# Optimization experiments

Measured on AMD Instinct MI355X. Metric: run time of the kernel, lower is better.

## Reference

```python
import jax, jax.numpy as jnp
import numpy as np

N_NODES = 100000
N_EDGES = 1_600_000
F_IN, HID, N_CLS = 128, 64, 32
NEG_SLOPE = 0.2  # PyG GATv2Conv default


def _segment_softmax(scores, seg, num_segments):
    # numerically stable softmax over edges grouped by destination node
    m = jax.ops.segment_max(scores, seg, num_segments=num_segments)
    ex = jnp.exp(scores - m[seg])
    s = jax.ops.segment_sum(ex, seg, num_segments=num_segments)
    return ex / (s[seg] + 1e-16)


def _gatv2_layer(x, src, dst, Wl, bl, Wr, br, att, bias, num_nodes):
    xl = x @ Wl + bl              # source transform  [N, C]
    xr = x @ Wr + br              # target transform  [N, C]
    # per-edge GATv2 attention logit: a . leaky_relu(xl_j + xr_i)
    e = jax.nn.leaky_relu(xl[src] + xr[dst], NEG_SLOPE) @ att  # [E]
    alpha = _segment_softmax(e, dst, num_nodes)                 # [E]
    out = jax.ops.segment_sum(alpha[:, None] * xl[src], dst, num_segments=num_nodes)
    return out + bias


def _add_self_loops(edge_index, n):
    loops = jnp.arange(n, dtype=edge_index.dtype)
    return jnp.concatenate([edge_index, jnp.stack([loops, loops])], axis=1)


def setup_inputs() -> dict:
    key = jax.random.key(0)
    ks = jax.random.split(key, 8)
    s1 = 1.0 / np.sqrt(F_IN)
    s2 = 1.0 / np.sqrt(HID)
    return {
        "x": jax.random.normal(ks[0], (N_NODES, F_IN), jnp.float32),
        "edge_index": jax.random.randint(ks[1], (2, N_EDGES), 0, N_NODES, jnp.int64),
        "W1l": jax.random.normal(ks[2], (F_IN, HID), jnp.float32) * s1,
        "b1l": jnp.zeros((HID,), jnp.float32),
        "W1r": jax.random.normal(ks[3], (F_IN, HID), jnp.float32) * s1,
        "b1r": jnp.zeros((HID,), jnp.float32),
        "att1": jax.random.normal(ks[4], (HID,), jnp.float32) * s2,
        "bias1": jnp.zeros((HID,), jnp.float32),
        "W2l": jax.random.normal(ks[5], (HID, N_CLS), jnp.float32) * s2,
        "b2l": jnp.zeros((N_CLS,), jnp.float32),
        "W2r": jax.random.normal(ks[6], (HID, N_CLS), jnp.float32) * s2,
        "b2r": jnp.zeros((N_CLS,), jnp.float32),
        "att2": jax.random.normal(ks[7], (N_CLS,), jnp.float32) / np.sqrt(N_CLS),
        "bias2": jnp.zeros((N_CLS,), jnp.float32),
    }


def reference(x, edge_index, W1l, b1l, W1r, b1r, att1, bias1,
              W2l, b2l, W2r, b2r, att2, bias2):
    n = x.shape[0]
    ei = _add_self_loops(edge_index, n)
    src, dst = ei[0], ei[1]
    h = jax.nn.relu(_gatv2_layer(x, src, dst, W1l, b1l, W1r, b1r, att1, bias1, n))
    # F.dropout(training=False) is identity in eval mode
    out = _gatv2_layer(h, src, dst, W2l, b2l, W2r, b2r, att2, bias2, n)
    return out
```

## Files before the change

kernel.cpp:

```cpp
#include <hip/hip_runtime.h>
#include <hip/hip_fp16.h>
#include <math.h>

#define F_IN 128
#define HID 64
#define NCLS 32
#define NEG 0.2f
#define NBKT 128
#define BSH 7
#define BMSK 127
#define CHUNK 4096

using bf8 = __attribute__((ext_vector_type(8))) short;
using f4v = __attribute__((ext_vector_type(4))) float;
typedef _Float16 hv2 __attribute__((ext_vector_type(2)));

__device__ __forceinline__ void f4fma(float4& a, float s, const float4& w) {
    a.x = fmaf(s, w.x, a.x);
    a.y = fmaf(s, w.y, a.y);
    a.z = fmaf(s, w.z, a.z);
    a.w = fmaf(s, w.w, a.w);
}
__device__ __forceinline__ unsigned short f2bf(float f) {
    unsigned u = __float_as_uint(f);
    return (unsigned short)((u + 0x7FFFu + ((u >> 16) & 1u)) >> 16);
}
__device__ __forceinline__ unsigned short f2h(float f) {
    return __half_as_ushort(__float2half(f));
}
__device__ __forceinline__ float h2f(unsigned short u) {
    return __half2float(__ushort_as_half(u));
}
__device__ __forceinline__ unsigned pkaddabs(unsigned a, unsigned b) {
    hv2 r = __builtin_bit_cast(hv2, a) + __builtin_bit_cast(hv2, b);
    return __builtin_bit_cast(unsigned, r) & 0x7FFF7FFFu;
}
__device__ __forceinline__ float fdot2(unsigned a, unsigned b, float c) {
    return __builtin_amdgcn_fdot2(__builtin_bit_cast(hv2, a),
                                  __builtin_bit_cast(hv2, b), c, false);
}
__device__ __forceinline__ float h2lo(unsigned a) {
    return (float)__builtin_bit_cast(hv2, a).x;
}
__device__ __forceinline__ float h2hi(unsigned a) {
    return (float)__builtin_bit_cast(hv2, a).y;
}
template <int CTRL>
__device__ __forceinline__ float dpp_add(float v) {
    int t = __builtin_amdgcn_update_dpp(0, __float_as_int(v), CTRL, 0xf, 0xf, true);
    return v + __int_as_float(t);
}


__global__ __launch_bounds__(256) void bucketHist(const int* __restrict__ ei,
                                                  int Eorig, int Etot,
                                                  int* __restrict__ bucketSize, int BK) {
    __shared__ int h[1024];
    int t = threadIdx.x;
    for (int j = t; j < BK; j += 256) h[j] = 0;
    __syncthreads();
    int base = blockIdx.x * CHUNK;
    int end = base + CHUNK < Etot ? base + CHUNK : Etot;
    for (int i = base + t; i < end; i += 256) {
        int dst = i < Eorig ? ei[Eorig + i] : i - Eorig;
        atomicAdd(&h[dst >> BSH], 1);
    }
    __syncthreads();
    for (int j = t; j < BK; j += 256)
        if (h[j]) atomicAdd(&bucketSize[j], h[j]);
}

__global__ __launch_bounds__(256) void bucketScan(const int* __restrict__ bucketSize,
                                                  int* __restrict__ bucketStart,
                                                  int* __restrict__ bucketCursor,
                                                  int BK, int Etot) {
    __shared__ int sd[256];
    int t = threadIdx.x;
    int v[4]; int ts = 0;
#pragma unroll
    for (int k = 0; k < 4; k++) {
        v[k] = (4 * t + k < BK) ? bucketSize[4 * t + k] : 0;
        ts += v[k];
    }
    sd[t] = ts;
    __syncthreads();
    for (int off = 1; off < 256; off <<= 1) {
        int x = (t >= off) ? sd[t - off] : 0;
        __syncthreads();
        sd[t] += x;
        __syncthreads();
    }
    int excl = sd[t] - ts;
#pragma unroll
    for (int k = 0; k < 4; k++) {
        if (4 * t + k < BK) { bucketStart[4 * t + k] = excl; bucketCursor[4 * t + k] = excl; }
        excl += v[k];
    }
    if (t == 255) bucketStart[BK] = Etot;
}

__global__ __launch_bounds__(256) void bucketScatter(const int* __restrict__ ei,
                                                     int Eorig, int Etot,
                                                     int* __restrict__ bucketCursor,
                                                     int* __restrict__ pairs, int BK) {
    __shared__ int h[1024], lbase[1024], hcur[1024];
    int t = threadIdx.x;
    for (int j = t; j < BK; j += 256) { h[j] = 0; hcur[j] = 0; }
    __syncthreads();
    int base = blockIdx.x * CHUNK;
    int end = base + CHUNK < Etot ? base + CHUNK : Etot;
    for (int i = base + t; i < end; i += 256) {
        int dst = i < Eorig ? ei[Eorig + i] : i - Eorig;
        atomicAdd(&h[dst >> BSH], 1);
    }
    __syncthreads();
    for (int j = t; j < BK; j += 256)
        lbase[j] = h[j] ? atomicAdd(&bucketCursor[j], h[j]) : 0;
    __syncthreads();
    for (int i = base + t; i < end; i += 256) {
        int src, dst;
        if (i < Eorig) { src = ei[i]; dst = ei[Eorig + i]; }
        else           { src = dst = i - Eorig; }
        int b = dst >> BSH;
        int off = atomicAdd(&hcur[b], 1);
        pairs[lbase[b] + off] = (src << BSH) | (dst & BMSK);
    }
}

__global__ __launch_bounds__(256) void bucketCSR(const int* __restrict__ pairs,
                                                 const int* __restrict__ bucketStart,
                                                 int* __restrict__ rowstart,
                                                 int* __restrict__ cnt,
                                                 int* __restrict__ srclist, int N) {
    __shared__ int c[256], cur[256];
    int t = threadIdx.x;
    int b = blockIdx.x;
    int lo = b * NBKT;
    int eb = bucketStart[b], ee = bucketStart[b + 1];
    c[t] = 0;
    __syncthreads();
    for (int i = eb + t; i < ee; i += 256)
        atomicAdd(&c[pairs[i] & BMSK], 1);
    __syncthreads();
    cur[t] = c[t];
    __syncthreads();
    for (int off = 1; off < 256; off <<= 1) {
        int x = (t >= off) ? cur[t - off] : 0;
        __syncthreads();
        cur[t] += x;
        __syncthreads();
    }
    int excl = cur[t] - c[t];
    int node = lo + t;
    if (t < NBKT && node < N) { rowstart[node] = eb + excl; cnt[node] = c[t]; }
    __syncthreads();
    cur[t] = excl;
    __syncthreads();
    for (int i = eb + t; i < ee; i += 256) {
        int v = pairs[i];
        int pos = atomicAdd(&cur[v & BMSK], 1);
        srclist[eb + pos] = v >> BSH;
    }
}

__global__ __launch_bounds__(256) void prepW(const float* __restrict__ Wl,
                                             const float* __restrict__ Wr,
                                             const float* __restrict__ att1,
                                             const float* __restrict__ att2,
                                             uint4* __restrict__ wfrag,
                                             unsigned short* __restrict__ att1h,
                                             unsigned short* __restrict__ att2h) {
    int e = blockIdx.x * 256 + threadIdx.x;
    if (e >= 2048) {
        int i = e - 2048;
        if (i < HID) att1h[i] = f2h(att1[i]);
        else if (i < HID + NCLS) att2h[i - HID] = f2h(att2[i - HID]);
        return;
    }
    int lane = e & 63;
    int kt = (e >> 6) & 3;
    int ct = (e >> 8) & 3;
    int mat = e >> 10;
    const float* W = mat ? Wr : Wl;
    int k0 = kt * 32 + (lane >> 4) * 8;
    int c = ct * 16 + (lane & 15);
    unsigned short h[8];
#pragma unroll
    for (int j = 0; j < 8; j++) h[j] = f2bf(W[(k0 + j) * HID + c]);
    wfrag[e] = *(uint4*)h;
}

__global__ __launch_bounds__(256) void transform1(const float* __restrict__ x,
                                                  const uint4* __restrict__ wfrag,
                                                  const float* __restrict__ bl,
                                                  const float* __restrict__ br,
                                                  const float* __restrict__ att,
                                                  unsigned short* __restrict__ xlh,
                                                  unsigned short* __restrict__ xrh,
                                                  float* __restrict__ sl, int N) {
    __shared__ uint4 sw[2048];
    int t = threadIdx.x;
#pragma unroll
    for (int j = 0; j < 8; j++) sw[t + j * 256] = wfrag[t + j * 256];
    __syncthreads();

    int w = t >> 6, lane = t & 63;
    int nb = blockIdx.x * 64 + w * 16;
    int m = lane & 15, quad = lane >> 4;

    int arow = nb + m; if (arow >= N) arow = N - 1;
    const float* xrow = x + (size_t)arow * F_IN + quad * 8;
    bf8 afr[4];
#pragma unroll
    for (int kt = 0; kt < 4; kt++) {
        float4 lo = *(const float4*)(xrow + kt * 32);
        float4 hi = *(const float4*)(xrow + kt * 32 + 4);
        unsigned short hh[8];
        hh[0] = f2bf(lo.x); hh[1] = f2bf(lo.y); hh[2] = f2bf(lo.z); hh[3] = f2bf(lo.w);
        hh[4] = f2bf(hi.x); hh[5] = f2bf(hi.y); hh[6] = f2bf(hi.z); hh[7] = f2bf(hi.w);
        afr[kt] = *(bf8*)hh;
    }

    float am[4];
#pragma unroll
    for (int ct = 0; ct < 4; ct++) am[ct] = att[ct * 16 + m];
    float slp[4] = {0.f, 0.f, 0.f, 0.f};

#pragma unroll
    for (int mat = 0; mat < 2; mat++) {
        const float* bias = mat ? br : bl;
#pragma unroll
        for (int ct = 0; ct < 4; ct++) {
            f4v acc = {0.f, 0.f, 0.f, 0.f};
#pragma unroll
            for (int kt = 0; kt < 4; kt++) {
                bf8 bfr = *(bf8*)&sw[((mat * 4 + ct) * 4 + kt) * 64 + lane];
                acc = __builtin_amdgcn_mfma_f32_16x16x32_bf16(afr[kt], bfr, acc, 0, 0, 0);
            }
            int ch = ct * 16 + m;
            float bv = bias[ch];
#pragma unroll
            for (int reg = 0; reg < 4; reg++) {
                int node = nb + quad * 4 + reg;
                float o = acc[reg] + bv;
                if (mat) {
                    if (node < N) xrh[(size_t)node * HID + ch] = f2h(o);
                } else {
                    unsigned short hb = f2h(o);
                    slp[reg] = fmaf(am[ct], h2f(hb), slp[reg]);
                    if (node < N) xlh[(size_t)node * HID + ch] = hb;
                }
            }
        }
    }
#pragma unroll
    for (int reg = 0; reg < 4; reg++) {
        slp[reg] = dpp_add<0xB1>(slp[reg]);
        slp[reg] = dpp_add<0x4E>(slp[reg]);
        slp[reg] = dpp_add<0x141>(slp[reg]);
        slp[reg] = dpp_add<0x140>(slp[reg]);
    }
    if (m == 0) {
#pragma unroll
        for (int reg = 0; reg < 4; reg++) {
            int node = nb + quad * 4 + reg;
            if (node < N) sl[node] = 0.6f * slp[reg];
        }
    }
}

__global__ __launch_bounds__(256) void transform2(const float* __restrict__ h,
                                                  const float* __restrict__ Wl,
                                                  const float* __restrict__ bl,
                                                  const float* __restrict__ Wr,
                                                  const float* __restrict__ br,
                                                  const float* __restrict__ att,
                                                  unsigned short* __restrict__ xlh,
                                                  unsigned short* __restrict__ xrh,
                                                  float* __restrict__ sl, int N) {
    __shared__ float sWl[HID * NCLS];
    __shared__ float sWr[HID * NCLS];
    __shared__ float sx[128][68];
    int t = threadIdx.x;
    int nb = blockIdx.x * 128;

#pragma unroll
    for (int j = 0; j < 2; j++) {
        int f = t + j * 256;
        ((float4*)sWl)[f] = ((const float4*)Wl)[f];
        ((float4*)sWr)[f] = ((const float4*)Wr)[f];
    }
    int maxf = (N - nb) * 16;
#pragma unroll
    for (int j = 0; j < 8; j++) {
        int f = t + j * 256;
        int node = f >> 4, kc = f & 15;
        float4 v = {0.f, 0.f, 0.f, 0.f};
        if (f < maxf) v = ((const float4*)(h + (size_t)nb * HID))[f];
        v.x = fmaxf(v.x, 0.f);
        v.y = fmaxf(v.y, 0.f);
        v.z = fmaxf(v.z, 0.f);
        v.w = fmaxf(v.w, 0.f);
        *(float4*)&sx[node][kc * 4] = v;
    }
    __syncthreads();

    int c4 = (t & 7) * 4;
    int slot = t >> 3;
    float4 bl4 = *(const float4*)(bl + c4);
    float4 br4 = *(const float4*)(br + c4);
    float4 at4 = *(const float4*)(att + c4);
    float4 accl[4] = {bl4, bl4, bl4, bl4};
    float4 accr[4] = {br4, br4, br4, br4};

#pragma unroll 4
    for (int k4 = 0; k4 < HID / 4; k4++) {
        int k = k4 * 4;
        float4 wl0 = *(const float4*)&sWl[(k + 0) * NCLS + c4];
        float4 wl1 = *(const float4*)&sWl[(k + 1) * NCLS + c4];
        float4 wl2 = *(const float4*)&sWl[(k + 2) * NCLS + c4];
        float4 wl3 = *(const float4*)&sWl[(k + 3) * NCLS + c4];
        float4 wr0 = *(const float4*)&sWr[(k + 0) * NCLS + c4];
        float4 wr1 = *(const float4*)&sWr[(k + 1) * NCLS + c4];
        float4 wr2 = *(const float4*)&sWr[(k + 2) * NCLS + c4];
        float4 wr3 = *(const float4*)&sWr[(k + 3) * NCLS + c4];
#pragma unroll
        for (int j = 0; j < 4; j++) {
            float4 xv = *(const float4*)&sx[slot + j * 32][k];
            f4fma(accl[j], xv.x, wl0); f4fma(accr[j], xv.x, wr0);
            f4fma(accl[j], xv.y, wl1); f4fma(accr[j], xv.y, wr1);
            f4fma(accl[j], xv.z, wl2); f4fma(accr[j], xv.z, wr2);
            f4fma(accl[j], xv.w, wl3); f4fma(accr[j], xv.w, wr3);
        }
    }
#pragma unroll
    for (int j = 0; j < 4; j++) {
        ushort4 o;
        o.x = f2h(accl[j].x); o.y = f2h(accl[j].y);
        o.z = f2h(accl[j].z); o.w = f2h(accl[j].w);
        ushort4 orr;
        orr.x = f2h(accr[j].x); orr.y = f2h(accr[j].y);
        orr.z = f2h(accr[j].z); orr.w = f2h(accr[j].w);
        float slpj = fmaf(at4.x, h2f(o.x),
                     fmaf(at4.y, h2f(o.y),
                     fmaf(at4.z, h2f(o.z), at4.w * h2f(o.w))));
        slpj = dpp_add<0xB1>(slpj);
        slpj = dpp_add<0x4E>(slpj);
        slpj = dpp_add<0x141>(slpj);
        int g = nb + slot + j * 32;
        if (g < N) {
            *(ushort4*)(xlh + (size_t)g * NCLS + c4) = o;
            *(ushort4*)(xrh + (size_t)g * NCLS + c4) = orr;
            if ((t & 7) == 0) sl[g] = 0.6f * slpj;
        }
    }
}

#define LOADROW(VP, SRC)                                                  \
    {                                                                     \
        const unsigned short* rp = xlh + (unsigned)(SRC) * C + cb0;       \
        if (NH == 4) *(uint4*)(VP) = *(const uint4*)rp;                   \
        else         *(uint2*)(VP) = *(const uint2*)rp;                   \
    }

#define COMPUTE(VP, T, B)                                                 \
    {                                                                     \
        float pa = 0.f;                                                   \
        _Pragma("unroll")                                                 \
        for (int j = 0; j < NH; j++)                                      \
            pa = fdot2(pkaddabs((VP)[j], xrp[j]), atp[j], pa);            \
        pa = dpp_add<0x128>(pa);                                          \
        pa += __shfl_xor(pa, 16, 64);                                     \
        pa += __shfl_xor(pa, 32, 64);                                     \
        float wgt = ((B) * 8 + slot < len) ? __expf(fmaf(0.4f, pa, (T)))  \
                                           : 0.f;                         \
        s += wgt;                                                         \
        _Pragma("unroll")                                                 \
        for (int j = 0; j < NH; j++) {                                    \
            acc[2 * j]     = fmaf(wgt, h2lo((VP)[j]), acc[2 * j]);        \
            acc[2 * j + 1] = fmaf(wgt, h2hi((VP)[j]), acc[2 * j + 1]);    \
        }                                                                 \
    }

template <int C>
__global__ __launch_bounds__(256) void fusedAggG(const unsigned short* __restrict__ xlh,
                                                 const unsigned short* __restrict__ xrh,
                                                 const unsigned short* __restrict__ atth,
                                                 const float* __restrict__ sl,
                                                 const int* __restrict__ rowstart,
                                                 const int* __restrict__ cnt,
                                                 const int* __restrict__ srclist,
                                                 const float* __restrict__ bias,
                                                 float* __restrict__ out, int N) {
    constexpr int CH = C / 8;
    constexpr int NH = CH / 2;
    int wid = threadIdx.x >> 6;
    int lane = threadIdx.x & 63;
    int n = blockIdx.x * 4 + wid;
    if (n >= N) return;

    int slot = lane & 7;
    int pos  = lane >> 3;
    int cb0  = pos * CH;

    unsigned xrp[NH], atp[NH];
    if (NH == 4) {
        *(uint4*)xrp = *(const uint4*)(xrh + (size_t)n * C + cb0);
        *(uint4*)atp = *(const uint4*)(atth + cb0);
    } else {
        *(uint2*)xrp = *(const uint2*)(xrh + (size_t)n * C + cb0);
        *(uint2*)atp = *(const uint2*)(atth + cb0);
    }

    int row = rowstart[n];
    int deg = cnt[n];

    float s = 0.f;
    float acc[CH];
#pragma unroll
    for (int c = 0; c < CH; c++) acc[c] = 0.f;

    for (int cb = 0; cb < deg; cb += 64) {
        int len = deg - cb; if (len > 64) len = 64;
        int len1 = len - 1;
        int li = lane < len ? lane : len1;
        int srcv = srclist[row + cb + li];
        float slv = sl[srcv];
        int nbatch = (len + 7) >> 3;

        float tA = __shfl(slv, slot, 64);
        int srcA = __shfl(srcv, slot, 64);
        unsigned vpA[NH], vpB[NH];
        float tB;
        LOADROW(vpA, srcA)

        int b = 0;
        while (true) {
            bool moreB = (b + 1 < nbatch);
            if (moreB) {
                int e = (b + 1) * 8 + slot;
                tB = __shfl(slv, e, 64);
                int srcB = __shfl(srcv, e, 64);
                LOADROW(vpB, srcB)
            }
            COMPUTE(vpA, tA, b)
            if (!moreB) break;
            bool moreA = (b + 2 < nbatch);
            if (moreA) {
                int e = (b + 2) * 8 + slot;
                tA = __shfl(slv, e, 64);
                int srcA2 = __shfl(srcv, e, 64);
                LOADROW(vpA, srcA2)
            }
            COMPUTE(vpB, tB, b + 1)
            if (!moreA) break;
            b += 2;
        }
    }
#pragma unroll
    for (int c = 0; c < CH; c++) {
        acc[c] = dpp_add<0xB1>(acc[c]);
        acc[c] = dpp_add<0x4E>(acc[c]);
        acc[c] = dpp_add<0x141>(acc[c]);
    }
    s = dpp_add<0xB1>(s);
    s = dpp_add<0x4E>(s);
    s = dpp_add<0x141>(s);

    if (slot == 0) {
        float inv = 1.f / (s + 1e-16f);
        float o8[CH];
        float bi[CH];
        if (NH == 4) {
            *(float4*)&bi[0] = *(const float4*)(bias + cb0);
            *(float4*)&bi[4] = *(const float4*)(bias + cb0 + 4);
        } else {
            *(float4*)&bi[0] = *(const float4*)(bias + cb0);
        }
#pragma unroll
        for (int c = 0; c < CH; c++) o8[c] = fmaf(acc[c], inv, bi[c]);
        if (NH == 4) {
            *(float4*)(out + (size_t)n * C + cb0)     = *(float4*)&o8[0];
            *(float4*)(out + (size_t)n * C + cb0 + 4) = *(float4*)&o8[4];
        } else {
            *(float4*)(out + (size_t)n * C + cb0) = *(float4*)&o8[0];
        }
    }
}

extern "C" void kernel_launch(void* const* d_in, const int* in_sizes, int n_in,
                              void* d_out, int out_size, void* d_ws, size_t ws_size,
                              hipStream_t stream) {
    const float* x     = (const float*)d_in[0];
    const int*   ei    = (const int*)d_in[1];
    const float* W1l   = (const float*)d_in[2];
    const float* b1l   = (const float*)d_in[3];
    const float* W1r   = (const float*)d_in[4];
    const float* b1r   = (const float*)d_in[5];
    const float* att1  = (const float*)d_in[6];
    const float* bias1 = (const float*)d_in[7];
    const float* W2l   = (const float*)d_in[8];
    const float* b2l   = (const float*)d_in[9];
    const float* W2r   = (const float*)d_in[10];
    const float* b2r   = (const float*)d_in[11];
    const float* att2  = (const float*)d_in[12];
    const float* bias2 = (const float*)d_in[13];
    float* out = (float*)d_out;

    int N     = in_sizes[0] / F_IN;
    int Eorig = in_sizes[1] / 2;
    int Etot  = Eorig + N;
    int BK    = (N + NBKT - 1) / NBKT;

    char* p = (char*)d_ws;
    auto alloc = [&](size_t bytes) { void* r = (void*)p; p += (bytes + 255) & ~(size_t)255; return r; };
    unsigned short* xl1h = (unsigned short*)alloc((size_t)N * HID * 2);
    unsigned short* xr1h = (unsigned short*)alloc((size_t)N * HID * 2);
    float* h       = (float*)alloc((size_t)N * HID * 4);
    unsigned short* xl2h = (unsigned short*)alloc((size_t)N * NCLS * 2);
    unsigned short* xr2h = (unsigned short*)alloc((size_t)N * NCLS * 2);
    int*   cnt     = (int*)alloc((size_t)N * 4);
    int*   rowstart= (int*)alloc((size_t)N * 4);
    int*   srclist = (int*)alloc((size_t)Etot * 4);
    uint4* wfrag   = (uint4*)alloc(2048 * 16);
    float* sl1     = (float*)alloc((size_t)N * 4);
    float* sl2     = (float*)alloc((size_t)N * 4);
    unsigned short* att1h = (unsigned short*)alloc(HID * 2);
    unsigned short* att2h = (unsigned short*)alloc(NCLS * 2);
    int*   bucketSize   = (int*)alloc(1040 * 4);
    int*   bucketStart  = (int*)alloc(1040 * 4);
    int*   bucketCursor = (int*)alloc(1040 * 4);
    int*   pairs   = (int*)h;

    int nChunks = (Etot + CHUNK - 1) / CHUNK;

    hipMemsetAsync(bucketSize, 0, 1040 * 4, stream);
    bucketHist<<<nChunks, 256, 0, stream>>>(ei, Eorig, Etot, bucketSize, BK);
    bucketScan<<<1, 256, 0, stream>>>(bucketSize, bucketStart, bucketCursor, BK, Etot);
    bucketScatter<<<nChunks, 256, 0, stream>>>(ei, Eorig, Etot, bucketCursor, pairs, BK);
    bucketCSR<<<BK, 256, 0, stream>>>(pairs, bucketStart, rowstart, cnt, srclist, N);

    prepW<<<9, 256, 0, stream>>>(W1l, W1r, att1, att2, wfrag, att1h, att2h);
    transform1<<<(N + 63) / 64, 256, 0, stream>>>(x, wfrag, b1l, b1r, att1, xl1h, xr1h, sl1, N);
    fusedAggG<HID><<<(N + 3) / 4, 256, 0, stream>>>(xl1h, xr1h, att1h, sl1, rowstart, cnt,
                                                    srclist, bias1, h, N);

    transform2<<<(N + 127) / 128, 256, 0, stream>>>(h, W2l, b2l, W2r, b2r, att2, xl2h, xr2h, sl2, N);
    fusedAggG<NCLS><<<(N + 3) / 4, 256, 0, stream>>>(xl2h, xr2h, att2h, sl2, rowstart, cnt,
                                                     srclist, bias2, out, N);
}
```

Baseline: 298.9 us.

## Scatter edges into fixed-capacity buckets and deepen gather prefetch to four batches

Replaces the two-pass histogram-then-scatter bucket build with a single pass that atomically appends each edge into a fixed-capacity padded bucket (4096 slots per bucket), removing one read pass over the edge list and the cursor array. The CSR builder now reads each bucket from its padded region. The aggregation kernel's software pipeline goes from double to quadruple buffering of neighbor rows, putting more gathers in flight. The padded buckets assume no bucket exceeds 4096 edges, which holds only for the uniform random degree distribution (about 2176 per bucket) and risks overflow on skewed graphs. Global atomics per edge also add contention.

Result: slower. 714.6 us (+139.1%).

```diff
diff --git a/kernel.cpp b/kernel.cpp
--- a/kernel.cpp
+++ b/kernel.cpp
@@ -9,7 +9,7 @@
 #define NBKT 128
 #define BSH 7
 #define BMSK 127
-#define CHUNK 4096
+#define BCAPSH 12
 
 using bf8 = __attribute__((ext_vector_type(8))) short;
 using f4v = __attribute__((ext_vector_type(4))) float;
@@ -52,27 +52,22 @@
 }
 
 
-__global__ __launch_bounds__(256) void bucketHist(const int* __restrict__ ei,
+__global__ __launch_bounds__(256) void scatterPad(const int* __restrict__ ei,
                                                   int Eorig, int Etot,
-                                                  int* __restrict__ bucketSize, int BK) {
-    __shared__ int h[1024];
-    int t = threadIdx.x;
-    for (int j = t; j < BK; j += 256) h[j] = 0;
-    __syncthreads();
-    int base = blockIdx.x * CHUNK;
-    int end = base + CHUNK < Etot ? base + CHUNK : Etot;
-    for (int i = base + t; i < end; i += 256) {
-        int dst = i < Eorig ? ei[Eorig + i] : i - Eorig;
-        atomicAdd(&h[dst >> BSH], 1);
-    }
-    __syncthreads();
-    for (int j = t; j < BK; j += 256)
-        if (h[j]) atomicAdd(&bucketSize[j], h[j]);
+                                                  int* __restrict__ bucketSize,
+                                                  int* __restrict__ pairs) {
+    int i = blockIdx.x * 256 + threadIdx.x;
+    if (i >= Etot) return;
+    int src, dst;
+    if (i < Eorig) { src = ei[i]; dst = ei[Eorig + i]; }
+    else           { src = dst = i - Eorig; }
+    int b = dst >> BSH;
+    int off = atomicAdd(&bucketSize[b], 1);
+    pairs[(b << BCAPSH) + off] = (src << BSH) | (dst & BMSK);
 }
 
 __global__ __launch_bounds__(256) void bucketScan(const int* __restrict__ bucketSize,
                                                   int* __restrict__ bucketStart,
-                                                  int* __restrict__ bucketCursor,
                                                   int BK, int Etot) {
     __shared__ int sd[256];
     int t = threadIdx.x;
@@ -93,38 +88,10 @@
     int excl = sd[t] - ts;
 #pragma unroll
     for (int k = 0; k < 4; k++) {
-        if (4 * t + k < BK) { bucketStart[4 * t + k] = excl; bucketCursor[4 * t + k] = excl; }
+        if (4 * t + k < BK) bucketStart[4 * t + k] = excl;
         excl += v[k];
     }
     if (t == 255) bucketStart[BK] = Etot;
-}
-
-__global__ __launch_bounds__(256) void bucketScatter(const int* __restrict__ ei,
-                                                     int Eorig, int Etot,
-                                                     int* __restrict__ bucketCursor,
-                                                     int* __restrict__ pairs, int BK) {
-    __shared__ int h[1024], lbase[1024], hcur[1024];
-    int t = threadIdx.x;
-    for (int j = t; j < BK; j += 256) { h[j] = 0; hcur[j] = 0; }
-    __syncthreads();
-    int base = blockIdx.x * CHUNK;
-    int end = base + CHUNK < Etot ? base + CHUNK : Etot;
-    for (int i = base + t; i < end; i += 256) {
-        int dst = i < Eorig ? ei[Eorig + i] : i - Eorig;
-        atomicAdd(&h[dst >> BSH], 1);
-    }
-    __syncthreads();
-    for (int j = t; j < BK; j += 256)
-        lbase[j] = h[j] ? atomicAdd(&bucketCursor[j], h[j]) : 0;
-    __syncthreads();
-    for (int i = base + t; i < end; i += 256) {
-        int src, dst;
-        if (i < Eorig) { src = ei[i]; dst = ei[Eorig + i]; }
-        else           { src = dst = i - Eorig; }
-        int b = dst >> BSH;
-        int off = atomicAdd(&hcur[b], 1);
-        pairs[lbase[b] + off] = (src << BSH) | (dst & BMSK);
-    }
 }
 
 __global__ __launch_bounds__(256) void bucketCSR(const int* __restrict__ pairs,
@@ -136,11 +103,13 @@
     int t = threadIdx.x;
     int b = blockIdx.x;
     int lo = b * NBKT;
-    int eb = bucketStart[b], ee = bucketStart[b + 1];
+    int eb = bucketStart[b];
+    int ecount = bucketStart[b + 1] - eb;
+    const int* bp = pairs + ((size_t)b << BCAPSH);
     c[t] = 0;
     __syncthreads();
-    for (int i = eb + t; i < ee; i += 256)
-        atomicAdd(&c[pairs[i] & BMSK], 1);
+    for (int i = t; i < ecount; i += 256)
+        atomicAdd(&c[bp[i] & BMSK], 1);
     __syncthreads();
     cur[t] = c[t];
     __syncthreads();
@@ -156,8 +125,8 @@
     __syncthreads();
     cur[t] = excl;
     __syncthreads();
-    for (int i = eb + t; i < ee; i += 256) {
-        int v = pairs[i];
+    for (int i = t; i < ecount; i += 256) {
+        int v = bp[i];
         int pos = atomicAdd(&cur[v & BMSK], 1);
         srclist[eb + pos] = v >> BSH;
     }
@@ -363,6 +332,14 @@
         else         *(uint2*)(VP) = *(const uint2*)rp;                   \
     }
 
+#define LOADB(VP, T, B)                                                   \
+    {                                                                     \
+        int e_ = (B) * 8 + slot;                                          \
+        T = __shfl(slv, e_, 64);                                          \
+        int s_ = __shfl(srcv, e_, 64);                                    \
+        LOADROW(VP, s_)                                                   \
+    }
+
 #define COMPUTE(VP, T, B)                                                 \
     {                                                                     \
         float pa = 0.f;                                                   \
@@ -383,7 +360,7 @@
     }
 
 template <int C>
-__global__ __launch_bounds__(256) void fusedAggG(const unsigned short* __restrict__ xlh,
+__global__ __launch_bounds__(256) void fusedAggH(const unsigned short* __restrict__ xlh,
                                                  const unsigned short* __restrict__ xrh,
                                                  const unsigned short* __restrict__ atth,
                                                  const float* __restrict__ sl,
@@ -428,33 +405,27 @@
         float slv = sl[srcv];
         int nbatch = (len + 7) >> 3;
 
-        float tA = __shfl(slv, slot, 64);
-        int srcA = __shfl(srcv, slot, 64);
-        unsigned vpA[NH], vpB[NH];
-        float tB;
-        LOADROW(vpA, srcA)
+        unsigned vp0[NH], vp1[NH], vp2[NH], vp3[NH];
+        float t0, t1, t2, t3;
+        LOADB(vp0, t0, 0)
+        if (nbatch > 1) LOADB(vp1, t1, 1)
+        if (nbatch > 2) LOADB(vp2, t2, 2)
 
         int b = 0;
         while (true) {
-            bool moreB = (b + 1 < nbatch);
-            if (moreB) {
-                int e = (b + 1) * 8 + slot;
-                tB = __shfl(slv, e, 64);
-                int srcB = __shfl(srcv, e, 64);
-                LOADROW(vpB, srcB)
-            }
-            COMPUTE(vpA, tA, b)
-            if (!moreB) break;
-            bool moreA = (b + 2 < nbatch);
-            if (moreA) {
-                int e = (b + 2) * 8 + slot;
-                tA = __shfl(slv, e, 64);
-                int srcA2 = __shfl(srcv, e, 64);
-                LOADROW(vpA, srcA2)
-            }
-            COMPUTE(vpB, tB, b + 1)
-            if (!moreA) break;
-            b += 2;
+            if (b + 3 < nbatch) LOADB(vp3, t3, b + 3)
+            COMPUTE(vp0, t0, b)
+            if (b + 1 >= nbatch) break;
+            if (b + 4 < nbatch) LOADB(vp0, t0, b + 4)
+            COMPUTE(vp1, t1, b + 1)
+            if (b + 2 >= nbatch) break;
+            if (b + 5 < nbatch) LOADB(vp1, t1, b + 5)
+            COMPUTE(vp2, t2, b + 2)
+            if (b + 3 >= nbatch) break;
+            if (b + 6 < nbatch) LOADB(vp2, t2, b + 6)
+            COMPUTE(vp3, t3, b + 3)
+            if (b + 4 >= nbatch) break;
+            b += 4;
         }
     }
 #pragma unroll
@@ -529,23 +500,19 @@
     unsigned short* att2h = (unsigned short*)alloc(NCLS * 2);
     int*   bucketSize   = (int*)alloc(1040 * 4);
     int*   bucketStart  = (int*)alloc(1040 * 4);
-    int*   bucketCursor = (int*)alloc(1040 * 4);
     int*   pairs   = (int*)h;
 
-    int nChunks = (Etot + CHUNK - 1) / CHUNK;
-
     hipMemsetAsync(bucketSize, 0, 1040 * 4, stream);
-    bucketHist<<<nChunks, 256, 0, stream>>>(ei, Eorig, Etot, bucketSize, BK);
-    bucketScan<<<1, 256, 0, stream>>>(bucketSize, bucketStart, bucketCursor, BK, Etot);
-    bucketScatter<<<nChunks, 256, 0, stream>>>(ei, Eorig, Etot, bucketCursor, pairs, BK);
+    scatterPad<<<(Etot + 255) / 256, 256, 0, stream>>>(ei, Eorig, Etot, bucketSize, pairs);
+    bucketScan<<<1, 256, 0, stream>>>(bucketSize, bucketStart, BK, Etot);
     bucketCSR<<<BK, 256, 0, stream>>>(pairs, bucketStart, rowstart, cnt, srclist, N);
 
     prepW<<<9, 256, 0, stream>>>(W1l, W1r, att1, att2, wfrag, att1h, att2h);
     transform1<<<(N + 63) / 64, 256, 0, stream>>>(x, wfrag, b1l, b1r, att1, xl1h, xr1h, sl1, N);
-    fusedAggG<HID><<<(N + 3) / 4, 256, 0, stream>>>(xl1h, xr1h, att1h, sl1, rowstart, cnt,
+    fusedAggH<HID><<<(N + 3) / 4, 256, 0, stream>>>(xl1h, xr1h, att1h, sl1, rowstart, cnt,
                                                     srclist, bias1, h, N);
 
     transform2<<<(N + 127) / 128, 256, 0, stream>>>(h, W2l, b2l, W2r, b2r, att2, xl2h, xr2h, sl2, N);
-    fusedAggG<NCLS><<<(N + 3) / 4, 256, 0, stream>>>(xl2h, xr2h, att2h, sl2, rowstart, cnt,
+    fusedAggH<NCLS><<<(N + 3) / 4, 256, 0, stream>>>(xl2h, xr2h, att2h, sl2, rowstart, cnt,
                                                      srclist, bias2, out, N);
 }
```

## Merge weight prep into histogram and transform1 into scatter kernel launches

Applied to the files above, without the earlier changes.

Folds the prepW blocks into the bucket histogram kernel, and the transform1 blocks into the bucket scatter kernel, by giving each combined launch extra blocks that branch on blockIdx. This removes two kernel launches and lets the independent dense transform overlap with the edge scatter on the GPU. The scatter path now reuses the 32KB uint4 shared buffer for its three 1024-int arrays. The merged kernel carries the larger register and shared footprint of whichever role is heavier, which may lower occupancy for the scatter blocks.

Result: no change. 302.0 us (+1.0%).

```diff
diff --git a/kernel.cpp b/kernel.cpp
--- a/kernel.cpp
+++ b/kernel.cpp
@@ -52,11 +52,51 @@
 }
 
 
-__global__ __launch_bounds__(256) void bucketHist(const int* __restrict__ ei,
-                                                  int Eorig, int Etot,
-                                                  int* __restrict__ bucketSize, int BK) {
+__device__ __forceinline__ void prepW_body(int pb, int t,
+                                           const float* __restrict__ Wl,
+                                           const float* __restrict__ Wr,
+                                           const float* __restrict__ att1,
+                                           const float* __restrict__ att2,
+                                           uint4* __restrict__ wfrag,
+                                           unsigned short* __restrict__ att1h,
+                                           unsigned short* __restrict__ att2h) {
+    int e = pb * 256 + t;
+    if (e >= 2048) {
+        int i = e - 2048;
+        if (i < HID) att1h[i] = f2h(att1[i]);
+        else if (i < HID + NCLS) att2h[i - HID] = f2h(att2[i - HID]);
+        return;
+    }
+    int lane = e & 63;
+    int kt = (e >> 6) & 3;
+    int ct = (e >> 8) & 3;
+    int mat = e >> 10;
+    const float* W = mat ? Wr : Wl;
+    int k0 = kt * 32 + (lane >> 4) * 8;
+    int c = ct * 16 + (lane & 15);
+    unsigned short h[8];
+#pragma unroll
+    for (int j = 0; j < 8; j++) h[j] = f2bf(W[(k0 + j) * HID + c]);
+    wfrag[e] = *(uint4*)h;
+}
+
+__global__ __launch_bounds__(256) void histPrep(const int* __restrict__ ei,
+                                                int Eorig, int Etot,
+                                                int* __restrict__ bucketSize, int BK,
+                                                int nChunks,
+                                                const float* __restrict__ Wl,
+                                                const float* __restrict__ Wr,
+                                                const float* __restrict__ att1,
+                                                const float* __restrict__ att2,
+                                                uint4* __restrict__ wfrag,
+                                                unsigned short* __restrict__ att1h,
+                                                unsigned short* __restrict__ att2h) {
     __shared__ int h[1024];
     int t = threadIdx.x;
+    if ((int)blockIdx.x >= nChunks) {
+        prepW_body(blockIdx.x - nChunks, t, Wl, Wr, att1, att2, wfrag, att1h, att2h);
+        return;
+    }
     for (int j = t; j < BK; j += 256) h[j] = 0;
     __syncthreads();
     int base = blockIdx.x * CHUNK;
@@ -99,12 +139,107 @@
     if (t == 255) bucketStart[BK] = Etot;
 }
 
-__global__ __launch_bounds__(256) void bucketScatter(const int* __restrict__ ei,
-                                                     int Eorig, int Etot,
-                                                     int* __restrict__ bucketCursor,
-                                                     int* __restrict__ pairs, int BK) {
-    __shared__ int h[1024], lbase[1024], hcur[1024];
+__device__ __forceinline__ void transform1_body(int tb, int t, uint4* sw,
+                                                const float* __restrict__ x,
+                                                const uint4* __restrict__ wfrag,
+                                                const float* __restrict__ bl,
+                                                const float* __restrict__ br,
+                                                const float* __restrict__ att,
+                                                unsigned short* __restrict__ xlh,
+                                                unsigned short* __restrict__ xrh,
+                                                float* __restrict__ sl, int N) {
+#pragma unroll
+    for (int j = 0; j < 8; j++) sw[t + j * 256] = wfrag[t + j * 256];
+    __syncthreads();
+
+    int w = t >> 6, lane = t & 63;
+    int nb = tb * 64 + w * 16;
+    int m = lane & 15, quad = lane >> 4;
+
+    int arow = nb + m; if (arow >= N) arow = N - 1;
+    const float* xrow = x + (size_t)arow * F_IN + quad * 8;
+    bf8 afr[4];
+#pragma unroll
+    for (int kt = 0; kt < 4; kt++) {
+        float4 lo = *(const float4*)(xrow + kt * 32);
+        float4 hi = *(const float4*)(xrow + kt * 32 + 4);
+        unsigned short hh[8];
+        hh[0] = f2bf(lo.x); hh[1] = f2bf(lo.y); hh[2] = f2bf(lo.z); hh[3] = f2bf(lo.w);
+        hh[4] = f2bf(hi.x); hh[5] = f2bf(hi.y); hh[6] = f2bf(hi.z); hh[7] = f2bf(hi.w);
+        afr[kt] = *(bf8*)hh;
+    }
+
+    float am[4];
+#pragma unroll
+    for (int ct = 0; ct < 4; ct++) am[ct] = att[ct * 16 + m];
+    float slp[4] = {0.f, 0.f, 0.f, 0.f};
+
+#pragma unroll
+    for (int mat = 0; mat < 2; mat++) {
+        const float* bias = mat ? br : bl;
+#pragma unroll
+        for (int ct = 0; ct < 4; ct++) {
+            f4v acc = {0.f, 0.f, 0.f, 0.f};
+#pragma unroll
+            for (int kt = 0; kt < 4; kt++) {
+                bf8 bfr = *(bf8*)&sw[((mat * 4 + ct) * 4 + kt) * 64 + lane];
+                acc = __builtin_amdgcn_mfma_f32_16x16x32_bf16(afr[kt], bfr, acc, 0, 0, 0);
+            }
+            int ch = ct * 16 + m;
+            float bv = bias[ch];
+#pragma unroll
+            for (int reg = 0; reg < 4; reg++) {
+                int node = nb + quad * 4 + reg;
+                float o = acc[reg] + bv;
+                if (mat) {
+                    if (node < N) xrh[(size_t)node * HID + ch] = f2h(o);
+                } else {
+                    unsigned short hb = f2h(o);
+                    slp[reg] = fmaf(am[ct], h2f(hb), slp[reg]);
+                    if (node < N) xlh[(size_t)node * HID + ch] = hb;
+                }
+            }
+        }
+    }
+#pragma unroll
+    for (int reg = 0; reg < 4; reg++) {
+        slp[reg] = dpp_add<0xB1>(slp[reg]);
+        slp[reg] = dpp_add<0x4E>(slp[reg]);
+        slp[reg] = dpp_add<0x141>(slp[reg]);
+        slp[reg] = dpp_add<0x140>(slp[reg]);
+    }
+    if (m == 0) {
+#pragma unroll
+        for (int reg = 0; reg < 4; reg++) {
+            int node = nb + quad * 4 + reg;
+            if (node < N) sl[node] = 0.6f * slp[reg];
+        }
+    }
+}
+
+__global__ __launch_bounds__(256) void scatT1(const int* __restrict__ ei,
+                                              int Eorig, int Etot,
+                                              int* __restrict__ bucketCursor,
+                                              int* __restrict__ pairs, int BK,
+                                              int nChunks,
+                                              const float* __restrict__ x,
+                                              const uint4* __restrict__ wfrag,
+                                              const float* __restrict__ bl,
+                                              const float* __restrict__ br,
+                                              const float* __restrict__ att,
+                                              unsigned short* __restrict__ xlh,
+                                              unsigned short* __restrict__ xrh,
+                                              float* __restrict__ sl, int N) {
+    __shared__ uint4 sw[2048];
     int t = threadIdx.x;
+    if ((int)blockIdx.x >= nChunks) {
+        transform1_body(blockIdx.x - nChunks, t, sw, x, wfrag, bl, br, att,
+                        xlh, xrh, sl, N);
+        return;
+    }
+    int* h     = (int*)sw;
+    int* lbase = h + 1024;
+    int* hcur  = h + 2048;
     for (int j = t; j < BK; j += 256) { h[j] = 0; hcur[j] = 0; }
     __syncthreads();
     int base = blockIdx.x * CHUNK;
@@ -160,112 +295,6 @@
         int v = pairs[i];
         int pos = atomicAdd(&cur[v & BMSK], 1);
         srclist[eb + pos] = v >> BSH;
-    }
-}
-
-__global__ __launch_bounds__(256) void prepW(const float* __restrict__ Wl,
-                                             const float* __restrict__ Wr,
-                                             const float* __restrict__ att1,
-                                             const float* __restrict__ att2,
-                                             uint4* __restrict__ wfrag,
-                                             unsigned short* __restrict__ att1h,
-                                             unsigned short* __restrict__ att2h) {
-    int e = blockIdx.x * 256 + threadIdx.x;
-    if (e >= 2048) {
-        int i = e - 2048;
-        if (i < HID) att1h[i] = f2h(att1[i]);
-        else if (i < HID + NCLS) att2h[i - HID] = f2h(att2[i - HID]);
-        return;
-    }
-    int lane = e & 63;
-    int kt = (e >> 6) & 3;
-    int ct = (e >> 8) & 3;
-    int mat = e >> 10;
-    const float* W = mat ? Wr : Wl;
-    int k0 = kt * 32 + (lane >> 4) * 8;
-    int c = ct * 16 + (lane & 15);
-    unsigned short h[8];
-#pragma unroll
-    for (int j = 0; j < 8; j++) h[j] = f2bf(W[(k0 + j) * HID + c]);
-    wfrag[e] = *(uint4*)h;
-}
-
-__global__ __launch_bounds__(256) void transform1(const float* __restrict__ x,
-                                                  const uint4* __restrict__ wfrag,
-                                                  const float* __restrict__ bl,
-                                                  const float* __restrict__ br,
-                                                  const float* __restrict__ att,
-                                                  unsigned short* __restrict__ xlh,
-                                                  unsigned short* __restrict__ xrh,
-                                                  float* __restrict__ sl, int N) {
-    __shared__ uint4 sw[2048];
-    int t = threadIdx.x;
-#pragma unroll
-    for (int j = 0; j < 8; j++) sw[t + j * 256] = wfrag[t + j * 256];
-    __syncthreads();
-
-    int w = t >> 6, lane = t & 63;
-    int nb = blockIdx.x * 64 + w * 16;
-    int m = lane & 15, quad = lane >> 4;
-
-    int arow = nb + m; if (arow >= N) arow = N - 1;
-    const float* xrow = x + (size_t)arow * F_IN + quad * 8;
-    bf8 afr[4];
-#pragma unroll
-    for (int kt = 0; kt < 4; kt++) {
-        float4 lo = *(const float4*)(xrow + kt * 32);
-        float4 hi = *(const float4*)(xrow + kt * 32 + 4);
-        unsigned short hh[8];
-        hh[0] = f2bf(lo.x); hh[1] = f2bf(lo.y); hh[2] = f2bf(lo.z); hh[3] = f2bf(lo.w);
-        hh[4] = f2bf(hi.x); hh[5] = f2bf(hi.y); hh[6] = f2bf(hi.z); hh[7] = f2bf(hi.w);
-        afr[kt] = *(bf8*)hh;
-    }
-
-    float am[4];
-#pragma unroll
-    for (int ct = 0; ct < 4; ct++) am[ct] = att[ct * 16 + m];
-    float slp[4] = {0.f, 0.f, 0.f, 0.f};
-
-#pragma unroll
-    for (int mat = 0; mat < 2; mat++) {
-        const float* bias = mat ? br : bl;
-#pragma unroll
-        for (int ct = 0; ct < 4; ct++) {
-            f4v acc = {0.f, 0.f, 0.f, 0.f};
-#pragma unroll
-            for (int kt = 0; kt < 4; kt++) {
-                bf8 bfr = *(bf8*)&sw[((mat * 4 + ct) * 4 + kt) * 64 + lane];
-                acc = __builtin_amdgcn_mfma_f32_16x16x32_bf16(afr[kt], bfr, acc, 0, 0, 0);
-            }
-            int ch = ct * 16 + m;
-            float bv = bias[ch];
-#pragma unroll
-            for (int reg = 0; reg < 4; reg++) {
-                int node = nb + quad * 4 + reg;
-                float o = acc[reg] + bv;
-                if (mat) {
-                    if (node < N) xrh[(size_t)node * HID + ch] = f2h(o);
-                } else {
-                    unsigned short hb = f2h(o);
-                    slp[reg] = fmaf(am[ct], h2f(hb), slp[reg]);
-                    if (node < N) xlh[(size_t)node * HID + ch] = hb;
-                }
-            }
-        }
-    }
-#pragma unroll
-    for (int reg = 0; reg < 4; reg++) {
-        slp[reg] = dpp_add<0xB1>(slp[reg]);
-        slp[reg] = dpp_add<0x4E>(slp[reg]);
-        slp[reg] = dpp_add<0x141>(slp[reg]);
-        slp[reg] = dpp_add<0x140>(slp[reg]);
-    }
-    if (m == 0) {
-#pragma unroll
-        for (int reg = 0; reg < 4; reg++) {
-            int node = nb + quad * 4 + reg;
-            if (node < N) sl[node] = 0.6f * slp[reg];
-        }
     }
 }
 
@@ -533,15 +562,17 @@
     int*   pairs   = (int*)h;
 
     int nChunks = (Etot + CHUNK - 1) / CHUNK;
+    int nT1     = (N + 63) / 64;
 
     hipMemsetAsync(bucketSize, 0, 1040 * 4, stream);
-    bucketHist<<<nChunks, 256, 0, stream>>>(ei, Eorig, Etot, bucketSize, BK);
+    histPrep<<<nChunks + 9, 256, 0, stream>>>(ei, Eorig, Etot, bucketSize, BK, nChunks,
+                                              W1l, W1r, att1, att2, wfrag, att1h, att2h);
     bucketScan<<<1, 256, 0, stream>>>(bucketSize, bucketStart, bucketCursor, BK, Etot);
-    bucketScatter<<<nChunks, 256, 0, stream>>>(ei, Eorig, Etot, bucketCursor, pairs, BK);
+    scatT1<<<nChunks + nT1, 256, 0, stream>>>(ei, Eorig, Etot, bucketCursor, pairs, BK,
+                                              nChunks, x, wfrag, b1l, b1r, att1,
+                                              xl1h, xr1h, sl1, N);
     bucketCSR<<<BK, 256, 0, stream>>>(pairs, bucketStart, rowstart, cnt, srclist, N);
 
-    prepW<<<9, 256, 0, stream>>>(W1l, W1r, att1, att2, wfrag, att1h, att2h);
-    transform1<<<(N + 63) / 64, 256, 0, stream>>>(x, wfrag, b1l, b1r, att1, xl1h, xr1h, sl1, N);
     fusedAggG<HID><<<(N + 3) / 4, 256, 0, stream>>>(xl1h, xr1h, att1h, sl1, rowstart, cnt,
                                                     srclist, bias1, h, N);
 
```
